# Kernel tuning notes

Measured on AMD Instinct MI355X. Metric: run time of the kernel, lower is better.

The kernel has to match this reference:

```python
import jax, jax.numpy as jnp
import numpy as np

U, I, D = 100000, 200000, 64   # users, items, emb_size
N = U + I                      # total nodes
NNZ = 6400000                  # adjacency non-zeros
B = 4096                       # batch of (user,item) pairs
L = 3                          # n_layers


def setup_inputs() -> dict:
    key = jax.random.key(0)
    ks = jax.random.split(key, 11)
    s = 1.0 / np.sqrt(D)  # xavier-ish scale
    return {
        "user_emb_online": jax.random.normal(ks[0], (U, D), jnp.float32) * s,
        "item_emb_online": jax.random.normal(ks[1], (I, D), jnp.float32) * s,
        "user_emb_target": jax.random.normal(ks[2], (U, D), jnp.float32) * s,
        "item_emb_target": jax.random.normal(ks[3], (I, D), jnp.float32) * s,
        # normalized adjacency values (positive, roughly 1/deg scale)
        "adj_val": jax.random.uniform(ks[4], (NNZ,), jnp.float32) * (1.0 / 16.0),
        "pred_w": jax.random.normal(ks[5], (D, D), jnp.float32) * s,
        "pred_b": jnp.zeros((D,), jnp.float32),
        "adj_row": jax.random.randint(ks[6], (NNZ,), 0, N, dtype=jnp.int32),
        "adj_col": jax.random.randint(ks[7], (NNZ,), 0, N, dtype=jnp.int32),
        "user_idx": jax.random.randint(ks[8], (B,), 0, U, dtype=jnp.int32),
        "item_idx": jax.random.randint(ks[9], (B,), 0, I, dtype=jnp.int32),
    }


def _spmm(row, col, val, x):
    # sparse [N,N] @ dense [N,D] via gather + segment-sum
    return jax.ops.segment_sum(val[:, None] * x[col], row, num_segments=N)


def _lgcn_encode(user_emb, item_emb, row, col, val):
    ego = jnp.concatenate([user_emb, item_emb], axis=0)  # [N, D]
    acc = ego
    x = ego
    for _ in range(L):
        x = _spmm(row, col, val, x)
        acc = acc + x
    all_emb = acc / (L + 1)  # mean over stacked layer outputs
    return all_emb[:U], all_emb[U:]


def reference(user_emb_online, item_emb_online, user_emb_target, item_emb_target,
              adj_val, pred_w, pred_b, adj_row, adj_col, user_idx, item_idx):
    u_on_all, i_on_all = _lgcn_encode(user_emb_online, item_emb_online, adj_row, adj_col, adj_val)
    u_tg_all, i_tg_all = _lgcn_encode(user_emb_target, item_emb_target, adj_row, adj_col, adj_val)
    u_online = u_on_all[user_idx]   # [B, D]
    i_online = i_on_all[item_idx]
    u_target = u_tg_all[user_idx]
    i_target = i_tg_all[item_idx]
    u_pred = u_online @ pred_w.T + pred_b  # nn.Linear
    i_pred = i_online @ pred_w.T + pred_b
    return (u_pred, u_target, i_pred, i_target)
```

## Files before the change

kernel.cpp:

```cpp
#include <hip/hip_runtime.h>
#include <hip/hip_bf16.h>
#include <stdint.h>

#define U_N   100000
#define I_N   200000
#define NN    300000
#define DD    64
#define NNZ_N 6400000
#define BB    4096
#define CHUNK 4096
#define NB    ((NN + CHUNK - 1) / CHUNK)
#define NBK   74
#define EPB   4096
#define NSB   1184
#define SUBCAP 6656
#define BKCAP  94208
#define BKBLK  23
#define LBLK   48000

typedef unsigned short u16;
typedef unsigned int   u32;
typedef float vf2 __attribute__((ext_vector_type(2)));

__device__ __forceinline__ u16 f2bf(float f) {
    u32 u = __float_as_uint(f);
    u32 r = (u + 0x7FFFu + ((u >> 16) & 1u)) >> 16;
    return (u16)r;
}


#if __has_builtin(__builtin_amdgcn_cvt_pk_f32_fp8) && __has_builtin(__builtin_amdgcn_cvt_pk_fp8_f32)
#define FP8_HW 1
#else
#define FP8_HW 0
#endif

__device__ __forceinline__ u32 enc1_fp8(float f) {
    float af = fabsf(f);
    u32 s = (__float_as_uint(f) >> 31) << 7;
    if (af >= 0.015625f) {
        u32 au = __float_as_uint(af);
        u32 r = au + 0x7FFFFu + ((au >> 20) & 1u);
        u32 e = (r >> 23) - 120u;
        u32 m = (r >> 20) & 7u;
        if (e > 15u) { e = 15u; m = 6u; }
        return s | (e << 3) | m;
    } else {
        u32 q = (u32)__float2int_rn(af * 512.0f);
        return s | q;
    }
}

__device__ __forceinline__ u32 pack4_fp8(float a, float b, float c, float d) {
#if FP8_HW
    u32 w = 0;
    w = (u32)__builtin_amdgcn_cvt_pk_fp8_f32(a, b, (int)w, false);
    w = (u32)__builtin_amdgcn_cvt_pk_fp8_f32(c, d, (int)w, true);
    return w;
#else
    return enc1_fp8(a) | (enc1_fp8(b) << 8) | (enc1_fp8(c) << 16) | (enc1_fp8(d) << 24);
#endif
}

__device__ __forceinline__ float dec1_fp8(u32 b) {
    u32 s = (b & 0x80u) << 24;
    u32 e = (b >> 3) & 15u;
    u32 m = b & 7u;
    float mag = e ? __uint_as_float(((e + 120u) << 23) | (m << 20))
                  : (float)m * 0.001953125f;
    return __uint_as_float(__float_as_uint(mag) | s);
}

__device__ __forceinline__ void dec_fp8x4(u32 w, float* f) {
#if FP8_HW
    vf2 lo = __builtin_amdgcn_cvt_pk_f32_fp8((int)w, false);
    vf2 hi = __builtin_amdgcn_cvt_pk_f32_fp8((int)w, true);
    f[0] = lo[0]; f[1] = lo[1]; f[2] = hi[0]; f[3] = hi[1];
#else
    f[0] = dec1_fp8(w & 255u); f[1] = dec1_fp8((w >> 8) & 255u);
    f[2] = dec1_fp8((w >> 16) & 255u); f[3] = dec1_fp8(w >> 24);
#endif
}


__global__ void binit_k(int* __restrict__ bkt_cursor) {
    int t = threadIdx.x;
    if (t < NBK) bkt_cursor[t] = t * BKCAP;
}


__global__ __launch_bounds__(256) void p1_k(const int* __restrict__ adj_row,
                                            const int* __restrict__ adj_col,
                                            const float* __restrict__ adj_val,
                                            int* __restrict__ bkt_cursor,
                                            u32* __restrict__ bpk,
                                            float* __restrict__ bval) {
    __shared__ int lcnt[NBK];
    __shared__ int lbase[NBK];
    int base = blockIdx.x * EPB;
    for (int i = threadIdx.x; i < NBK; i += 256) lcnt[i] = 0;
    __syncthreads();
    u32 pk[16]; float vv[16]; int bb[16]; int rk[16];
#pragma unroll
    for (int j = 0; j < 16; j++) {
        int e = base + j * 256 + threadIdx.x;
        bb[j] = -1;
        if (e < NNZ_N) {
            int r = adj_row[e];
            int c = adj_col[e];
            vv[j] = adj_val[e];
            int b = r >> 12;
            pk[j] = ((u32)(r & 4095) << 19) | (u32)c;
            bb[j] = b;
            rk[j] = atomicAdd(&lcnt[b], 1);
        }
    }
    __syncthreads();
    for (int i = threadIdx.x; i < NBK; i += 256)
        lbase[i] = atomicAdd(&bkt_cursor[i], lcnt[i]);
    __syncthreads();
#pragma unroll
    for (int j = 0; j < 16; j++) {
        if (bb[j] >= 0) {
            int p = lbase[bb[j]] + rk[j];
            bpk[p]  = pk[j];
            bval[p] = vv[j];
        }
    }
}


__global__ __launch_bounds__(1024) void bhist_k(const int* __restrict__ bkt_cursor,
                                                const u32* __restrict__ bpk,
                                                int* __restrict__ cnt) {
    __shared__ int h[4096];
    int b = blockIdx.x;
    int base = b * BKCAP;
    int e1 = bkt_cursor[b];
    for (int j = threadIdx.x; j < 4096; j += 1024) h[j] = 0;
    __syncthreads();
    for (int i = base + threadIdx.x; i < e1; i += 1024)
        atomicAdd(&h[bpk[i] >> 19], 1);
    __syncthreads();
    int rb = b << 12;
    for (int j = threadIdx.x; j < 4096; j += 1024) {
        int idx = rb + j;
        if (idx < NN) cnt[idx] = h[j];
    }
}


__global__ void scan1_k(const int* __restrict__ cnt, int* __restrict__ bsums) {
    __shared__ int red[256];
    int base = blockIdx.x * CHUNK;
    int s = 0;
    for (int j = threadIdx.x; j < CHUNK; j += 256) {
        int idx = base + j;
        s += (idx < NN) ? cnt[idx] : 0;
    }
    red[threadIdx.x] = s;
    __syncthreads();
    for (int o = 128; o > 0; o >>= 1) {
        if (threadIdx.x < o) red[threadIdx.x] += red[threadIdx.x + o];
        __syncthreads();
    }
    if (threadIdx.x == 0) bsums[blockIdx.x] = red[0];
}

__global__ void scan2_k(int* __restrict__ bsums, int* __restrict__ row_ptr) {
    __shared__ int sh[128];
    int v = (threadIdx.x < NB) ? bsums[threadIdx.x] : 0;
    sh[threadIdx.x] = v;
    __syncthreads();
    for (int o = 1; o < 128; o <<= 1) {
        int t = (threadIdx.x >= o) ? sh[threadIdx.x - o] : 0;
        __syncthreads();
        sh[threadIdx.x] += t;
        __syncthreads();
    }
    if (threadIdx.x < NB) bsums[threadIdx.x] = sh[threadIdx.x] - v;
    if (threadIdx.x == 127) row_ptr[NN] = sh[127];
}

__global__ void scan3_k(const int* __restrict__ cnt, const int* __restrict__ bsums,
                        int* __restrict__ row_ptr) {
    __shared__ int tsum[256];
    int base = blockIdx.x * CHUNK;
    int loc[16];
    int s = 0;
#pragma unroll
    for (int j = 0; j < 16; j++) {
        int idx = base + threadIdx.x * 16 + j;
        int c = (idx < NN) ? cnt[idx] : 0;
        loc[j] = s;
        s += c;
    }
    tsum[threadIdx.x] = s;
    __syncthreads();
    int v = s;
    for (int o = 1; o < 256; o <<= 1) {
        int t = (threadIdx.x >= o) ? tsum[threadIdx.x - o] : 0;
        __syncthreads();
        tsum[threadIdx.x] += t;
        __syncthreads();
    }
    int texcl = tsum[threadIdx.x] - v;
    int boff = bsums[blockIdx.x];
#pragma unroll
    for (int j = 0; j < 16; j++) {
        int idx = base + threadIdx.x * 16 + j;
        if (idx < NN) row_ptr[idx] = boff + texcl + loc[j];
    }
}

__global__ void subinit_k(const int* __restrict__ row_ptr, int* __restrict__ sub_cursor) {
    int s = blockIdx.x * blockDim.x + threadIdx.x;
    if (s < NSB) {
        int r = s << 8;
        sub_cursor[s] = row_ptr[(r < NN) ? r : NN];
    }
}


__global__ __launch_bounds__(256) void p2r_k(const int* __restrict__ bkt_cursor,
                                             const u32* __restrict__ bpk,
                                             const float* __restrict__ bval,
                                             int* __restrict__ sub_cursor,
                                             int2* __restrict__ mid) {
    __shared__ int lcnt[16], lbase[16], sbase[16];
    __shared__ int2 stage[4096];
    int b = blockIdx.y;
    int e1 = bkt_cursor[b];
    int base = b * BKCAP + blockIdx.x * 4096;
    if (base >= e1) return;
    if (threadIdx.x < 16) lcnt[threadIdx.x] = 0;
    __syncthreads();
    u32 pk[16]; float vv[16]; int sb[16], rk[16];
#pragma unroll
    for (int j = 0; j < 16; j++) {
        int e = base + j * 256 + threadIdx.x;
        sb[j] = -1;
        if (e < e1) {
            pk[j] = bpk[e];
            vv[j] = bval[e];
            int s = (int)((pk[j] >> 27) & 15u);
            sb[j] = s;
            rk[j] = atomicAdd(&lcnt[s], 1);
        }
    }
    __syncthreads();
    if (threadIdx.x == 0) {
        int acc = 0;
#pragma unroll
        for (int s = 0; s < 16; s++) { sbase[s] = acc; acc += lcnt[s]; }
    }
    if (threadIdx.x < 16)
        lbase[threadIdx.x] = atomicAdd(&sub_cursor[b * 16 + threadIdx.x], lcnt[threadIdx.x]);
    __syncthreads();
#pragma unroll
    for (int j = 0; j < 16; j++)
        if (sb[j] >= 0)
            stage[sbase[sb[j]] + rk[j]] = make_int2((int)pk[j], __float_as_int(vv[j]));
    __syncthreads();
    for (int s = 0; s < 16; s++) {
        int c = lcnt[s], gb = lbase[s], lb = sbase[s];
        for (int i = threadIdx.x; i < c; i += 256)
            mid[gb + i] = stage[lb + i];
    }
}


__global__ __launch_bounds__(256) void p3_k(const int* __restrict__ row_ptr,
                                            const int2* __restrict__ mid,
                                            int2* __restrict__ edge_s) {
    __shared__ int rbase[256], rcur[256];
    __shared__ int2 stage[SUBCAP];
    int s = blockIdx.x;
    int r0 = s << 8;
    if (r0 >= NN) return;
    int r1 = min(r0 + 256, NN);
    int nr = r1 - r0;
    int ebase = row_ptr[r0];
    int eend  = row_ptr[r1];
    int cnt = eend - ebase;
    if (threadIdx.x < nr) {
        rbase[threadIdx.x] = row_ptr[r0 + threadIdx.x] - ebase;
        rcur[threadIdx.x] = 0;
    }
    __syncthreads();
    for (int i = threadIdx.x; i < cnt; i += 256) {
        int2 d = mid[ebase + i];
        u32 pk = (u32)d.x;
        int l = (int)((pk >> 19) & 255u);
        int pos = rbase[l] + atomicAdd(&rcur[l], 1);
        if (pos < SUBCAP) stage[pos] = make_int2((int)(pk & 0x7FFFFu), d.y);
    }
    __syncthreads();
    for (int i = threadIdx.x; i < cnt; i += 256) edge_s[ebase + i] = stage[i];
}


__global__ void mark_k(const int* __restrict__ row_ptr, const int2* __restrict__ edge_s,
                       const int* __restrict__ user_idx, const int* __restrict__ item_idx,
                       unsigned char* __restrict__ mark) {
    int wave = threadIdx.x >> 6;
    int lane = threadIdx.x & 63;
    int slot = blockIdx.x * 4 + wave;
    if (slot >= 2 * BB) return;
    int r = (slot < BB) ? user_idx[slot] : U_N + item_idx[slot - BB];
    if (lane == 0) mark[r] = 1;
    int e0 = row_ptr[r], e1 = row_ptr[r + 1];
    for (int e = e0 + lane; e < e1; e += 64) mark[edge_s[e].x] = 1;
}

__global__ void compact_k(const unsigned char* __restrict__ mark,
                          int* __restrict__ list2, int* __restrict__ nlist) {
    int i = blockIdx.x * 256 + threadIdx.x;
    int lane = threadIdx.x & 63;
    int m = (i < NN) ? (int)mark[i] : 0;
    unsigned long long b = __ballot(m != 0);
    int pre = __popcll(b & ((1ull << lane) - 1ull));
    int tot = __popcll(b);
    int base = 0;
    if (lane == 0 && tot) base = atomicAdd(nlist, tot);
    base = __shfl(base, 0);
    if (m) list2[base + pre] = i;
}


__global__ void pack1_k(const float* __restrict__ ue_on, const float* __restrict__ ie_on,
                        const float* __restrict__ ue_tg, const float* __restrict__ ie_tg,
                        unsigned char* __restrict__ x0f) {
    int tid = blockIdx.x * blockDim.x + threadIdx.x;
    int n = tid >> 4;
    int t = tid & 15;
    if (n >= NN) return;
    const float* src;
    int soff;
    if (t < 8) {
        soff = t * 8;
        src = (n < U_N) ? ue_on + (size_t)n * 64 : ie_on + (size_t)(n - U_N) * 64;
    } else {
        soff = (t - 8) * 8;
        src = (n < U_N) ? ue_tg + (size_t)n * 64 : ie_tg + (size_t)(n - U_N) * 64;
    }
    float4 f0 = *(const float4*)(src + soff);
    float4 f1 = *(const float4*)(src + soff + 4);
    uint2 o;
    o.x = pack4_fp8(f0.x, f0.y, f0.z, f0.w);
    o.y = pack4_fp8(f1.x, f1.y, f1.z, f1.w);
    *(uint2*)(x0f + (size_t)n * 128 + t * 8) = o;
}


struct acc8 { float a[8]; };

__device__ __forceinline__ void red8(acc8& A) {
#pragma unroll
    for (int k = 0; k < 8; k++) {
        A.a[k] += __shfl_xor(A.a[k], 16);
        A.a[k] += __shfl_xor(A.a[k], 32);
    }
}

__global__ __launch_bounds__(256) void spmm1_k(const int* __restrict__ row_ptr,
                                               const int2* __restrict__ edge_s,
                                               const unsigned char* __restrict__ x0f,
                                               u16* __restrict__ y) {
    int lane = threadIdx.x & 63;
    int t = lane & 15, g = lane >> 4;
    int r = blockIdx.x * 4 + (threadIdx.x >> 6);
    if (r >= NN) return;
    int e0 = row_ptr[r], e1 = row_ptr[r + 1];
    int d = e1 - e0;
    acc8 A;
#pragma unroll
    for (int k = 0; k < 8; k++) A.a[k] = 0.f;
    const unsigned char* xt = x0f + t * 8;

    int2 ed[8];
    uint2 pv[8];
#pragma unroll
    for (int q = 0; q < 8; q++) { ed[q] = make_int2(0, 0); pv[q] = make_uint2(0u, 0u); }
#pragma unroll
    for (int q = 0; q < 8; q++) {
        int j = g + 4 * q;
        if (j < d) ed[q] = edge_s[e0 + j];
    }
#pragma unroll
    for (int q = 0; q < 8; q++) {
        int j = g + 4 * q;
        if (j < d) pv[q] = *(const uint2*)(xt + (size_t)(u32)ed[q].x * 128);
    }
#pragma unroll
    for (int q = 0; q < 8; q++) {
        float v = __int_as_float(ed[q].y);
        float f[8];
        dec_fp8x4(pv[q].x, f);
        dec_fp8x4(pv[q].y, f + 4);
#pragma unroll
        for (int k = 0; k < 8; k++) A.a[k] += v * f[k];
    }
    for (int e = e0 + 32 + g * 4; e < e1; e += 16) {
        int m = e1 - e;
#pragma unroll
        for (int k = 0; k < 4; k++) {
            if (k < m) {
                int2 dd = edge_s[e + k];
                float v = __int_as_float(dd.y);
                uint2 p = *(const uint2*)(xt + (size_t)(u32)dd.x * 128);
                float f[8];
                dec_fp8x4(p.x, f);
                dec_fp8x4(p.y, f + 4);
#pragma unroll
                for (int q = 0; q < 8; q++) A.a[q] += v * f[q];
            }
        }
    }
    red8(A);
    if (g == 0) {
        uint4 o;
        o.x = ((u32)f2bf(A.a[1]) << 16) | (u32)f2bf(A.a[0]);
        o.y = ((u32)f2bf(A.a[3]) << 16) | (u32)f2bf(A.a[2]);
        o.z = ((u32)f2bf(A.a[5]) << 16) | (u32)f2bf(A.a[4]);
        o.w = ((u32)f2bf(A.a[7]) << 16) | (u32)f2bf(A.a[6]);
        *(uint4*)(y + (size_t)r * 128 + t * 8) = o;
    }
}

__device__ __forceinline__ void rg16_core(const int2* __restrict__ edge_s,
                                          const u16* __restrict__ x,
                                          int t, int g, int e0, int e1, acc8& A) {
#pragma unroll
    for (int k = 0; k < 8; k++) A.a[k] = 0.f;
    const u16* xt = x + t * 8;
    int d = e1 - e0;

    int2 ed[8];
    uint4 pv[8];
#pragma unroll
    for (int q = 0; q < 8; q++) { ed[q] = make_int2(0, 0); pv[q] = make_uint4(0u, 0u, 0u, 0u); }
#pragma unroll
    for (int q = 0; q < 8; q++) {
        int j = g + 4 * q;
        if (j < d) ed[q] = edge_s[e0 + j];
    }
#pragma unroll
    for (int q = 0; q < 8; q++) {
        int j = g + 4 * q;
        if (j < d) pv[q] = *(const uint4*)(xt + (size_t)(u32)ed[q].x * 128);
    }
#pragma unroll
    for (int q = 0; q < 8; q++) {
        float v = __int_as_float(ed[q].y);
        A.a[0] += v * __uint_as_float(pv[q].x << 16);
        A.a[1] += v * __uint_as_float(pv[q].x & 0xFFFF0000u);
        A.a[2] += v * __uint_as_float(pv[q].y << 16);
        A.a[3] += v * __uint_as_float(pv[q].y & 0xFFFF0000u);
        A.a[4] += v * __uint_as_float(pv[q].z << 16);
        A.a[5] += v * __uint_as_float(pv[q].z & 0xFFFF0000u);
        A.a[6] += v * __uint_as_float(pv[q].w << 16);
        A.a[7] += v * __uint_as_float(pv[q].w & 0xFFFF0000u);
    }
    for (int e = e0 + 32 + g * 4; e < e1; e += 16) {
        int m = e1 - e;
#pragma unroll
        for (int k = 0; k < 4; k++) {
            if (k < m) {
                int2 dd = edge_s[e + k];
                float v = __int_as_float(dd.y);
                uint4 p = *(const uint4*)(xt + (size_t)(u32)dd.x * 128);
                A.a[0] += v * __uint_as_float(p.x << 16);
                A.a[1] += v * __uint_as_float(p.x & 0xFFFF0000u);
                A.a[2] += v * __uint_as_float(p.y << 16);
                A.a[3] += v * __uint_as_float(p.y & 0xFFFF0000u);
                A.a[4] += v * __uint_as_float(p.z << 16);
                A.a[5] += v * __uint_as_float(p.z & 0xFFFF0000u);
                A.a[6] += v * __uint_as_float(p.w << 16);
                A.a[7] += v * __uint_as_float(p.w & 0xFFFF0000u);
            }
        }
    }
    red8(A);
}

__global__ __launch_bounds__(256) void spmm_list_k(const int* __restrict__ row_ptr,
                                                   const int2* __restrict__ edge_s,
                                                   const u16* __restrict__ x,
                                                   u16* __restrict__ y,
                                                   const int* __restrict__ list2,
                                                   const int* __restrict__ nlist) {
    int lane = threadIdx.x & 63;
    int t = lane & 15, g = lane >> 4;
    int slot = blockIdx.x * 4 + (threadIdx.x >> 6);
    if (slot >= *nlist) return;
    int r = list2[slot];
    acc8 A;
    rg16_core(edge_s, x, t, g, row_ptr[r], row_ptr[r + 1], A);
    if (g == 0) {
        uint4 o;
        o.x = ((u32)f2bf(A.a[1]) << 16) | (u32)f2bf(A.a[0]);
        o.y = ((u32)f2bf(A.a[3]) << 16) | (u32)f2bf(A.a[2]);
        o.z = ((u32)f2bf(A.a[5]) << 16) | (u32)f2bf(A.a[4]);
        o.w = ((u32)f2bf(A.a[7]) << 16) | (u32)f2bf(A.a[6]);
        *(uint4*)(y + (size_t)r * 128 + t * 8) = o;
    }
}

__global__ __launch_bounds__(256) void spmm_last_k(const int* __restrict__ row_ptr,
                                                   const int2* __restrict__ edge_s,
                                                   const u16* __restrict__ x,
                                                   const int* __restrict__ user_idx,
                                                   const int* __restrict__ item_idx,
                                                   float* __restrict__ out_acc) {
    int lane = threadIdx.x & 63;
    int t = lane & 15, g = lane >> 4;
    int slot = blockIdx.x * 4 + (threadIdx.x >> 6);
    if (slot >= 2 * BB) return;
    int r = (slot < BB) ? user_idx[slot] : U_N + item_idx[slot - BB];
    acc8 A;
    rg16_core(edge_s, x, t, g, row_ptr[r], row_ptr[r + 1], A);
    if (g == 0) {
        float4* p0 = (float4*)(out_acc + (size_t)slot * 128 + t * 8);
        float4 c0 = p0[0], c1 = p0[1];
        c0.x += A.a[0]; c0.y += A.a[1]; c0.z += A.a[2]; c0.w += A.a[3];
        c1.x += A.a[4]; c1.y += A.a[5]; c1.z += A.a[6]; c1.w += A.a[7];
        p0[0] = c0; p0[1] = c1;
    }
}


__global__ void init_acc_k(const int* __restrict__ user_idx, const int* __restrict__ item_idx,
                           const float* __restrict__ ue_on, const float* __restrict__ ie_on,
                           const float* __restrict__ ue_tg, const float* __restrict__ ie_tg,
                           float* __restrict__ out_acc) {
    int t = blockIdx.x * blockDim.x + threadIdx.x;
    int slot = t >> 5;
    int j = t & 31;
    if (slot >= 2 * BB) return;
    int node = (slot < BB) ? user_idx[slot] : U_N + item_idx[slot - BB];
    const float* src;
    int soff, doff;
    if (j < 16) {
        soff = j * 4; doff = j * 4;
        src = (node < U_N) ? ue_on + (size_t)node * 64 : ie_on + (size_t)(node - U_N) * 64;
    } else {
        soff = (j - 16) * 4; doff = 64 + (j - 16) * 4;
        src = (node < U_N) ? ue_tg + (size_t)node * 64 : ie_tg + (size_t)(node - U_N) * 64;
    }
    float4 f = *(const float4*)(src + soff);
    *(float4*)(out_acc + (size_t)slot * 128 + doff) = f;
}

__global__ void gadd_k(const int* __restrict__ user_idx, const int* __restrict__ item_idx,
                       const u16* __restrict__ x, float* __restrict__ out_acc) {
    int t = blockIdx.x * blockDim.x + threadIdx.x;
    int slot = t >> 6;
    int l = t & 63;
    if (slot >= 2 * BB) return;
    int node = (slot < BB) ? user_idx[slot] : U_N + item_idx[slot - BB];
    u32 p = *(const u32*)(x + (size_t)node * 128 + (l << 1));
    float fx = __uint_as_float(p << 16);
    float fy = __uint_as_float(p & 0xFFFF0000u);
    float2* q = (float2*)(out_acc + (size_t)slot * 128) + l;
    float2 cur = *q;
    cur.x += fx; cur.y += fy;
    *q = cur;
}


__global__ __launch_bounds__(256) void pred_k(const float* __restrict__ out_acc,
                                              const float* __restrict__ W,
                                              const float* __restrict__ bias,
                                              float* __restrict__ out) {
    __shared__ float wld[64 * 65];
    __shared__ float uld[4 * 64];
    int j = threadIdx.x & 63;
    int rl = threadIdx.x >> 6;
    for (int i = threadIdx.x; i < 4096; i += 256) {
        int jj = i >> 6, kk = i & 63;
        wld[kk * 65 + jj] = W[i];
    }
    int slot = blockIdx.x * 4 + rl;
    uld[rl * 64 + j] = out_acc[(size_t)slot * 128 + j] * 0.25f;
    float tv = out_acc[(size_t)slot * 128 + 64 + j] * 0.25f;
    size_t tdst = (slot < BB) ? (size_t)BB * 64 + (size_t)slot * 64 + j
                              : (size_t)3 * BB * 64 + (size_t)(slot - BB) * 64 + j;
    out[tdst] = tv;
    __syncthreads();
    float acc = bias[j];
#pragma unroll
    for (int k = 0; k < 64; k++) acc += uld[rl * 64 + k] * wld[k * 65 + j];
    size_t dst = (slot < BB) ? (size_t)slot * 64 + j
                             : (size_t)2 * BB * 64 + (size_t)(slot - BB) * 64 + j;
    out[dst] = acc;
}


extern "C" void kernel_launch(void* const* d_in, const int* in_sizes, int n_in,
                              void* d_out, int out_size, void* d_ws, size_t ws_size,
                              hipStream_t stream) {
    const float* ue_on = (const float*)d_in[0];
    const float* ie_on = (const float*)d_in[1];
    const float* ue_tg = (const float*)d_in[2];
    const float* ie_tg = (const float*)d_in[3];
    const float* adj_val = (const float*)d_in[4];
    const float* pred_w = (const float*)d_in[5];
    const float* pred_b = (const float*)d_in[6];
    const int* adj_row = (const int*)d_in[7];
    const int* adj_col = (const int*)d_in[8];
    const int* user_idx = (const int*)d_in[9];
    const int* item_idx = (const int*)d_in[10];
    float* out = (float*)d_out;

    char* ws = (char*)d_ws;
    size_t off = 0;
    auto alloc = [&](size_t bytes) -> char* {
        char* p = ws + off;
        off = (off + bytes + 255) & ~(size_t)255;
        return p;
    };
    int*   cnt        = (int*)alloc((size_t)NN * 4);
    int*   row_ptr    = (int*)alloc((size_t)(NN + 1) * 4);
    int*   bsums      = (int*)alloc(256 * 4);
    int*   bkt_cursor = (int*)alloc(256 * 4);
    int*   sub_cursor = (int*)alloc((size_t)NSB * 4);
    unsigned char* mark = (unsigned char*)alloc((size_t)NN);
    int*   list2      = (int*)alloc((size_t)NN * 4);
    int*   nlist      = (int*)alloc(256 * 4);
    int2*  edge_s     = (int2*)alloc((size_t)NNZ_N * 8);
    u16*   x_a        = (u16*)alloc((size_t)NN * 128 * 2);
    u16*   x_b        = (u16*)alloc((size_t)NN * 128 * 2);
    float* out_acc    = (float*)alloc((size_t)2 * BB * 128 * 4);

    u32*   bpk  = (u32*)x_a;
    unsigned char* x0f = (unsigned char*)x_a;
    float* bval = (float*)x_b;
    int2*  mid  = edge_s;

    (void)n_in; (void)in_sizes; (void)out_size; (void)ws_size;

    hipMemsetAsync(mark, 0, (size_t)NN, stream);
    hipMemsetAsync(nlist, 0, 4, stream);
    binit_k<<<1, 128, 0, stream>>>(bkt_cursor);
    p1_k<<<(NNZ_N + EPB - 1) / EPB, 256, 0, stream>>>(adj_row, adj_col, adj_val, bkt_cursor, bpk, bval);
    bhist_k<<<NBK, 1024, 0, stream>>>(bkt_cursor, bpk, cnt);
    scan1_k<<<NB, 256, 0, stream>>>(cnt, bsums);
    scan2_k<<<1, 128, 0, stream>>>(bsums, row_ptr);
    scan3_k<<<NB, 256, 0, stream>>>(cnt, bsums, row_ptr);
    subinit_k<<<(NSB + 255) / 256, 256, 0, stream>>>(row_ptr, sub_cursor);
    p2r_k<<<dim3(BKBLK, NBK), 256, 0, stream>>>(bkt_cursor, bpk, bval, sub_cursor, mid);
    p3_k<<<NSB, 256, 0, stream>>>(row_ptr, mid, edge_s);

    mark_k<<<(2 * BB) / 4, 256, 0, stream>>>(row_ptr, edge_s, user_idx, item_idx, mark);
    compact_k<<<(NN + 255) / 256, 256, 0, stream>>>(mark, list2, nlist);

    pack1_k<<<(NN * 16 + 255) / 256, 256, 0, stream>>>(ue_on, ie_on, ue_tg, ie_tg, x0f);
    init_acc_k<<<(2 * BB * 32) / 256, 256, 0, stream>>>(user_idx, item_idx, ue_on, ie_on, ue_tg, ie_tg, out_acc);

    spmm1_k<<<NN / 4, 256, 0, stream>>>(row_ptr, edge_s, x0f, x_b);
    gadd_k<<<(2 * BB * 64) / 256, 256, 0, stream>>>(user_idx, item_idx, x_b, out_acc);
    spmm_list_k<<<LBLK, 256, 0, stream>>>(row_ptr, edge_s, x_b, x_a, list2, nlist);
    gadd_k<<<(2 * BB * 64) / 256, 256, 0, stream>>>(user_idx, item_idx, x_a, out_acc);
    spmm_last_k<<<(2 * BB) / 4, 256, 0, stream>>>(row_ptr, edge_s, x_a, user_idx, item_idx, out_acc);

    pred_k<<<(2 * BB) / 4, 256, 0, stream>>>(out_acc, pred_w, pred_b, out);
}
```

Before: 791.7 us.

## Fuse setup kernels, merge sub-cursor init into scan, two rows per wave

Replaces the two memsets and bucket-cursor init with a single setup kernel, and writes the sub-bucket cursors directly from the final scan so the separate init kernel is gone. The second gather-add is folded into the last SpMM kernel, which now adds the bf16 layer-2 value for its row before accumulating. The first SpMM processes two rows per wave so more independent gathers are in flight, at the cost of higher register use and possible load imbalance between the paired rows. These changes cut launch count and raise memory-level parallelism.

```diff
diff --git a/kernel.cpp b/kernel.cpp
--- a/kernel.cpp
+++ b/kernel.cpp
@@ -83,9 +83,12 @@
 }
 
 
-__global__ void binit_k(int* __restrict__ bkt_cursor) {
-    int t = threadIdx.x;
-    if (t < NBK) bkt_cursor[t] = t * BKCAP;
+__global__ void setup_k(unsigned char* __restrict__ mark, int* __restrict__ nlist,
+                        int* __restrict__ bkt_cursor) {
+    int tid = blockIdx.x * 256 + threadIdx.x;
+    if (tid < NN / 4) ((u32*)mark)[tid] = 0;
+    if (tid < NBK) bkt_cursor[tid] = tid * BKCAP;
+    if (tid == NN / 4) nlist[0] = 0;
 }
 
 
@@ -183,7 +186,7 @@
 }
 
 __global__ void scan3_k(const int* __restrict__ cnt, const int* __restrict__ bsums,
-                        int* __restrict__ row_ptr) {
+                        int* __restrict__ row_ptr, int* __restrict__ sub_cursor) {
     __shared__ int tsum[256];
     int base = blockIdx.x * CHUNK;
     int loc[16];
@@ -209,15 +212,11 @@
 #pragma unroll
     for (int j = 0; j < 16; j++) {
         int idx = base + threadIdx.x * 16 + j;
-        if (idx < NN) row_ptr[idx] = boff + texcl + loc[j];
-    }
-}
-
-__global__ void subinit_k(const int* __restrict__ row_ptr, int* __restrict__ sub_cursor) {
-    int s = blockIdx.x * blockDim.x + threadIdx.x;
-    if (s < NSB) {
-        int r = s << 8;
-        sub_cursor[s] = row_ptr[(r < NN) ? r : NN];
+        if (idx < NN) {
+            int val = boff + texcl + loc[j];
+            row_ptr[idx] = val;
+            if ((idx & 255) == 0) sub_cursor[idx >> 8] = val;
+        }
     }
 }
 
@@ -369,46 +368,69 @@
                                                u16* __restrict__ y) {
     int lane = threadIdx.x & 63;
     int t = lane & 15, g = lane >> 4;
-    int r = blockIdx.x * 4 + (threadIdx.x >> 6);
+    int r = blockIdx.x * 8 + (threadIdx.x >> 6) * 2;
     if (r >= NN) return;
-    int e0 = row_ptr[r], e1 = row_ptr[r + 1];
-    int d = e1 - e0;
-    acc8 A;
-#pragma unroll
-    for (int k = 0; k < 8; k++) A.a[k] = 0.f;
+    int e0a = row_ptr[r], e1a = row_ptr[r + 1], e1b = row_ptr[r + 2];
+    int e0b = e1a;
+    int da = e1a - e0a, db = e1b - e0b;
     const unsigned char* xt = x0f + t * 8;
 
-    int2 ed[8];
-    uint2 pv[8];
-#pragma unroll
-    for (int q = 0; q < 8; q++) { ed[q] = make_int2(0, 0); pv[q] = make_uint2(0u, 0u); }
+    int2 edA[8], edB[8];
+    uint2 pvA[8], pvB[8];
+#pragma unroll
+    for (int q = 0; q < 8; q++) {
+        edA[q] = make_int2(0, 0); edB[q] = make_int2(0, 0);
+        pvA[q] = make_uint2(0u, 0u); pvB[q] = make_uint2(0u, 0u);
+    }
 #pragma unroll
     for (int q = 0; q < 8; q++) {
         int j = g + 4 * q;
-        if (j < d) ed[q] = edge_s[e0 + j];
+        if (j < da) edA[q] = edge_s[e0a + j];
     }
 #pragma unroll
     for (int q = 0; q < 8; q++) {
         int j = g + 4 * q;
-        if (j < d) pv[q] = *(const uint2*)(xt + (size_t)(u32)ed[q].x * 128);
-    }
-#pragma unroll
-    for (int q = 0; q < 8; q++) {
-        float v = __int_as_float(ed[q].y);
+        if (j < db) edB[q] = edge_s[e0b + j];
+    }
+#pragma unroll
+    for (int q = 0; q < 8; q++) {
+        int j = g + 4 * q;
+        if (j < da) pvA[q] = *(const uint2*)(xt + (size_t)((u32)edA[q].x * 128u));
+    }
+#pragma unroll
+    for (int q = 0; q < 8; q++) {
+        int j = g + 4 * q;
+        if (j < db) pvB[q] = *(const uint2*)(xt + (size_t)((u32)edB[q].x * 128u));
+    }
+    acc8 A, B2;
+#pragma unroll
+    for (int k = 0; k < 8; k++) { A.a[k] = 0.f; B2.a[k] = 0.f; }
+#pragma unroll
+    for (int q = 0; q < 8; q++) {
+        float v = __int_as_float(edA[q].y);
         float f[8];
-        dec_fp8x4(pv[q].x, f);
-        dec_fp8x4(pv[q].y, f + 4);
+        dec_fp8x4(pvA[q].x, f);
+        dec_fp8x4(pvA[q].y, f + 4);
 #pragma unroll
         for (int k = 0; k < 8; k++) A.a[k] += v * f[k];
     }
-    for (int e = e0 + 32 + g * 4; e < e1; e += 16) {
-        int m = e1 - e;
+#pragma unroll
+    for (int q = 0; q < 8; q++) {
+        float v = __int_as_float(edB[q].y);
+        float f[8];
+        dec_fp8x4(pvB[q].x, f);
+        dec_fp8x4(pvB[q].y, f + 4);
+#pragma unroll
+        for (int k = 0; k < 8; k++) B2.a[k] += v * f[k];
+    }
+    for (int e = e0a + 32 + g * 4; e < e1a; e += 16) {
+        int m = e1a - e;
 #pragma unroll
         for (int k = 0; k < 4; k++) {
             if (k < m) {
                 int2 dd = edge_s[e + k];
                 float v = __int_as_float(dd.y);
-                uint2 p = *(const uint2*)(xt + (size_t)(u32)dd.x * 128);
+                uint2 p = *(const uint2*)(xt + (size_t)((u32)dd.x * 128u));
                 float f[8];
                 dec_fp8x4(p.x, f);
                 dec_fp8x4(p.y, f + 4);
@@ -417,7 +439,23 @@
             }
         }
     }
-    red8(A);
+    for (int e = e0b + 32 + g * 4; e < e1b; e += 16) {
+        int m = e1b - e;
+#pragma unroll
+        for (int k = 0; k < 4; k++) {
+            if (k < m) {
+                int2 dd = edge_s[e + k];
+                float v = __int_as_float(dd.y);
+                uint2 p = *(const uint2*)(xt + (size_t)((u32)dd.x * 128u));
+                float f[8];
+                dec_fp8x4(p.x, f);
+                dec_fp8x4(p.y, f + 4);
+#pragma unroll
+                for (int q = 0; q < 8; q++) B2.a[q] += v * f[q];
+            }
+        }
+    }
+    red8(A); red8(B2);
     if (g == 0) {
         uint4 o;
         o.x = ((u32)f2bf(A.a[1]) << 16) | (u32)f2bf(A.a[0]);
@@ -425,6 +463,12 @@
         o.z = ((u32)f2bf(A.a[5]) << 16) | (u32)f2bf(A.a[4]);
         o.w = ((u32)f2bf(A.a[7]) << 16) | (u32)f2bf(A.a[6]);
         *(uint4*)(y + (size_t)r * 128 + t * 8) = o;
+        uint4 o2;
+        o2.x = ((u32)f2bf(B2.a[1]) << 16) | (u32)f2bf(B2.a[0]);
+        o2.y = ((u32)f2bf(B2.a[3]) << 16) | (u32)f2bf(B2.a[2]);
+        o2.z = ((u32)f2bf(B2.a[5]) << 16) | (u32)f2bf(B2.a[4]);
+        o2.w = ((u32)f2bf(B2.a[7]) << 16) | (u32)f2bf(B2.a[6]);
+        *(uint4*)(y + (size_t)(r + 1) * 128 + t * 8) = o2;
     }
 }
 
@@ -521,6 +565,15 @@
     acc8 A;
     rg16_core(edge_s, x, t, g, row_ptr[r], row_ptr[r + 1], A);
     if (g == 0) {
+        uint4 p = *(const uint4*)(x + (size_t)r * 128 + t * 8);
+        A.a[0] += __uint_as_float(p.x << 16);
+        A.a[1] += __uint_as_float(p.x & 0xFFFF0000u);
+        A.a[2] += __uint_as_float(p.y << 16);
+        A.a[3] += __uint_as_float(p.y & 0xFFFF0000u);
+        A.a[4] += __uint_as_float(p.z << 16);
+        A.a[5] += __uint_as_float(p.z & 0xFFFF0000u);
+        A.a[6] += __uint_as_float(p.w << 16);
+        A.a[7] += __uint_as_float(p.w & 0xFFFF0000u);
         float4* p0 = (float4*)(out_acc + (size_t)slot * 128 + t * 8);
         float4 c0 = p0[0], c1 = p0[1];
         c0.x += A.a[0]; c0.y += A.a[1]; c0.z += A.a[2]; c0.w += A.a[3];
@@ -640,15 +693,12 @@
 
     (void)n_in; (void)in_sizes; (void)out_size; (void)ws_size;
 
-    hipMemsetAsync(mark, 0, (size_t)NN, stream);
-    hipMemsetAsync(nlist, 0, 4, stream);
-    binit_k<<<1, 128, 0, stream>>>(bkt_cursor);
+    setup_k<<<294, 256, 0, stream>>>(mark, nlist, bkt_cursor);
     p1_k<<<(NNZ_N + EPB - 1) / EPB, 256, 0, stream>>>(adj_row, adj_col, adj_val, bkt_cursor, bpk, bval);
     bhist_k<<<NBK, 1024, 0, stream>>>(bkt_cursor, bpk, cnt);
     scan1_k<<<NB, 256, 0, stream>>>(cnt, bsums);
     scan2_k<<<1, 128, 0, stream>>>(bsums, row_ptr);
-    scan3_k<<<NB, 256, 0, stream>>>(cnt, bsums, row_ptr);
-    subinit_k<<<(NSB + 255) / 256, 256, 0, stream>>>(row_ptr, sub_cursor);
+    scan3_k<<<NB, 256, 0, stream>>>(cnt, bsums, row_ptr, sub_cursor);
     p2r_k<<<dim3(BKBLK, NBK), 256, 0, stream>>>(bkt_cursor, bpk, bval, sub_cursor, mid);
     p3_k<<<NSB, 256, 0, stream>>>(row_ptr, mid, edge_s);
 
@@ -658,10 +708,9 @@
     pack1_k<<<(NN * 16 + 255) / 256, 256, 0, stream>>>(ue_on, ie_on, ue_tg, ie_tg, x0f);
     init_acc_k<<<(2 * BB * 32) / 256, 256, 0, stream>>>(user_idx, item_idx, ue_on, ie_on, ue_tg, ie_tg, out_acc);
 
-    spmm1_k<<<NN / 4, 256, 0, stream>>>(row_ptr, edge_s, x0f, x_b);
+    spmm1_k<<<NN / 8, 256, 0, stream>>>(row_ptr, edge_s, x0f, x_b);
     gadd_k<<<(2 * BB * 64) / 256, 256, 0, stream>>>(user_idx, item_idx, x_b, out_acc);
     spmm_list_k<<<LBLK, 256, 0, stream>>>(row_ptr, edge_s, x_b, x_a, list2, nlist);
-    gadd_k<<<(2 * BB * 64) / 256, 256, 0, stream>>>(user_idx, item_idx, x_a, out_acc);
     spmm_last_k<<<(2 * BB) / 4, 256, 0, stream>>>(row_ptr, edge_s, x_a, user_idx, item_idx, out_acc);
 
     pred_k<<<(2 * BB) / 4, 256, 0, stream>>>(out_acc, pred_w, pred_b, out);
```

After: 836.7 us. 5.7% more time.
